# Kernel optimization log

Hardware: AMD Instinct MI355X
Metric: run time of the kernel (lower is better)

Reference implementation:

```python
import jax, jax.numpy as jnp
import numpy as np
from jax import lax

S = 48          # fixed crop size (original crops are ragged; fixed here for batching)
EPS = 0.1       # Sinkhorn entropic regularization
ITERS = 50      # Sinkhorn iterations
TINY = 1e-8


def setup_inputs() -> dict:
    key = jax.random.key(0)
    k1, k2, k3 = jax.random.split(key, 3)
    B, C, H, W = 16, 5, 160, 160
    hm_gt = jax.random.uniform(k1, (B, C, H, W), dtype=jnp.float32)
    hm_pred = jax.random.uniform(k2, (B, C, H, W), dtype=jnp.float32)
    tops = jax.random.randint(k3, (B, 8, 2), 0, 112, dtype=jnp.int32)  # (y, x) per rect
    return {"hm_gt": hm_gt, "hm_pred": hm_pred, "tops": tops}


def _geometry_distance(s):
    # pairwise Euclidean distance between pixel centers of an s x s crop -> [s*s, s*s]
    ys, xs = jnp.meshgrid(jnp.arange(s, dtype=jnp.float32),
                          jnp.arange(s, dtype=jnp.float32), indexing="ij")
    pts = jnp.stack([ys.ravel(), xs.ravel()], axis=-1)          # [s*s, 2]
    d2 = jnp.sum((pts[:, None, :] - pts[None, :, :]) ** 2, -1)  # [s*s, s*s]
    return jnp.sqrt(d2)


def _crop_all(hm, tops):
    # hm: [B, C, H, W], tops: [B, R, 2] -> crops [B, R, C, S, S]
    def crop_one(hm_b, top):  # hm_b [C,H,W], top [2]
        return lax.dynamic_slice(hm_b, (0, top[0], top[1]), (hm_b.shape[0], S, S))
    return jax.vmap(lambda hb, tb: jax.vmap(lambda t: crop_one(hb, t))(tb))(hm, tops)


def reference(hm_gt, hm_pred, tops):
    B, C, H, W = hm_gt.shape
    n = S * S
    dist = _geometry_distance(S)            # [n, n]
    K = jnp.exp(-dist / EPS)                # Gibbs kernel
    M = K * dist                            # for the transport cost readout

    a = _crop_all(hm_gt, tops).reshape(-1, n)    # [N, n]
    b = _crop_all(hm_pred, tops).reshape(-1, n)  # [N, n]
    a = a / (jnp.sum(a, -1, keepdims=True) + TINY)   # normalize to marginals
    b = b / (jnp.sum(b, -1, keepdims=True) + TINY)

    N = a.shape[0]
    u0 = jnp.full((N, n), 1.0 / n, dtype=a.dtype)
    v0 = jnp.full((N, n), 1.0 / n, dtype=a.dtype)

    def body(carry, _):
        u, v = carry
        v = b / (u @ K + TINY)      # [N,n] @ [n,n]
        u = a / (v @ K.T + TINY)
        return (u, v), None

    (u, v), _ = lax.scan(body, (u0, v0), None, length=ITERS)
    # loss per crop: sum_ij u_i K_ij dist_ij v_j
    loss = jnp.sum((u @ M) * v)
    return loss
```

## Files before the change

kernel.cpp:

```cpp
#include <hip/hip_runtime.h>

#define TINYF 1e-8f
#define NITER 50

__device__ __forceinline__ float bperm(int addr4, float v) {
    return __int_as_float(__builtin_amdgcn_ds_bpermute(addr4, __float_as_int(v)));
}
__device__ __forceinline__ float dpp_shr1(float v) {
    return __int_as_float(__builtin_amdgcn_update_dpp(0, __float_as_int(v), 0x111, 0xf, 0xf, true));
}
__device__ __forceinline__ float dpp_shl1(float v) {
    return __int_as_float(__builtin_amdgcn_update_dpp(0, __float_as_int(v), 0x101, 0xf, 0xf, true));
}

#define PREPF(C0_, C1_, C2_) \
    L2 = dpp_shr1(C1_); L1 = dpp_shr1(C2_); R1 = dpp_shl1(C0_); R2 = dpp_shl1(C1_); \
    s1a = L1 + C1_; s1b = C0_ + C2_; s1c = C1_ + R1; \
    s2a = L2 + C2_; s2b = L1 + R1; s2c = C0_ + R2;
#define PREPS(C0_, C1_, C2_) \
    L1 = dpp_shr1(C2_); R1 = dpp_shl1(C0_); \
    s1a = L1 + C1_; s1b = C0_ + C2_; s1c = C1_ + R1;
#define AT0(I, C0_, C1_, C2_, KA, KB, KC) \
    acc[I][0] += KA * C0_ + KB * s1a + KC * s2a; \
    acc[I][1] += KA * C1_ + KB * s1b + KC * s2b; \
    acc[I][2] += KA * C2_ + KB * s1c + KC * s2c;
#define AT0I(I, C0_, C1_, C2_, KA, KB, KC) \
    acc[I][0] = KA * C0_ + KB * s1a + KC * s2a; \
    acc[I][1] = KA * C1_ + KB * s1b + KC * s2b; \
    acc[I][2] = KA * C2_ + KB * s1c + KC * s2c;
#define AT1(I, C0_, C1_, C2_, KA, KB) \
    acc[I][0] += KA * C0_ + KB * s1a; \
    acc[I][1] += KA * C1_ + KB * s1b; \
    acc[I][2] += KA * C2_ + KB * s1c;
#define AT1I(I, C0_, C1_, C2_, KA, KB) \
    acc[I][0] = KA * C0_ + KB * s1a; \
    acc[I][1] = KA * C1_ + KB * s1b; \
    acc[I][2] = KA * C2_ + KB * s1c;
#define AT2(I, C0_, C1_, C2_, KA) \
    acc[I][0] += KA * C0_; \
    acc[I][1] += KA * C1_; \
    acc[I][2] += KA * C2_;
#define AT2I(I, C0_, C1_, C2_, KA) \
    acc[I][0] = KA * C0_; \
    acc[I][1] = KA * C1_; \
    acc[I][2] = KA * C2_;

__global__ void __launch_bounds__(128)
__attribute__((amdgpu_waves_per_eu(1, 2)))
sinkhorn_ft(const float* __restrict__ hm_gt,
            const float* __restrict__ hm_pred,
            const int* __restrict__ tops,
            float* __restrict__ out) {
    __shared__ __align__(16) float EX[2 * 512];
    __shared__ float sred[4];

    const int t = threadIdx.x;
    const int W = t >> 6;
    const int l = t & 63;
    const int b = l >> 4, c = l & 15;
    const bool btop = (b == 0), bbot = (b == 3);
    const bool xchg = (W == 0) ? bbot : btop;
    const int upA = ((l - 16) & 63) << 2;
    const int dnA = ((l + 16) & 63) << 2;

    const int blk = blockIdx.x;
    const int bi = blk / 40, rr = (blk / 5) % 8, cc = blk % 5;
    const int y0 = tops[(bi * 8 + rr) * 2 + 0];
    const int x0 = tops[(bi * 8 + rr) * 2 + 1];
    const float* srcA = hm_gt + (size_t)(bi * 5 + cc) * 25600;
    const float* srcB = hm_pred + (size_t)(bi * 5 + cc) * 25600;

    float* wp = EX + W * 256 + c * 4;
    const float* rp = EX + (1 - W) * 256 + c * 4;

    float va[6][3], vb[6][3];
    float sA = 0.f, sB = 0.f;
    const int rbase = y0 + 24 * W + 6 * b;
#pragma unroll
    for (int i = 0; i < 6; ++i) {
        const int g = (rbase + i) * 160 + x0 + 3 * c;
#pragma unroll
        for (int j = 0; j < 3; ++j) {
            const float A = srcA[g + j];
            const float B = srcB[g + j];
            va[i][j] = A; vb[i][j] = B;
            sA += A; sB += B;
        }
    }
#pragma unroll
    for (int o = 1; o < 64; o <<= 1) {
        sA += __shfl_xor(sA, o, 64);
        sB += __shfl_xor(sB, o, 64);
    }
    if (l == 0) { sred[W] = sA; sred[2 + W] = sB; }
    __syncthreads();
    sA = sred[0] + sred[1];
    sB = sred[2] + sred[3];
    const float nA = 1.0f / (sA + TINYF);
    const float nB = 1.0f / (sB + TINYF);
#pragma unroll
    for (int i = 0; i < 6; ++i)
#pragma unroll
        for (int j = 0; j < 3; ++j) { va[i][j] *= nA; vb[i][j] *= nB; }

    const float e10 = expf(-1.0f / 0.1f);
    const float e2  = expf(-sqrtf(2.0f) / 0.1f);
    const float e20 = expf(-2.0f / 0.1f);

    float xu[6][3], xv[6][3], acc[6][3];
    const float u0 = 1.0f / 2304.0f;
#pragma unroll
    for (int i = 0; i < 6; ++i)
#pragma unroll
        for (int j = 0; j < 3; ++j) xu[i][j] = u0;

    if (xchg) {
        *(float4*)(wp)      = make_float4(u0, u0, u0, 0.f);
        *(float4*)(wp + 64) = make_float4(u0, u0, u0, 0.f);
    }
    __syncthreads();

    auto conv = [&](const float (&x)[6][3], int poffR,
                    float K00, float K01, float K02,
                    float K10, float K11, float K20) {
        float4 q0 = make_float4(0.f, 0.f, 0.f, 0.f), q1 = q0;
        if (xchg) {
            q0 = *(const float4*)(rp + poffR);
            q1 = *(const float4*)(rp + poffR + 64);
        }
        float tA[3], tB[3], tC[3], tD[3];
#pragma unroll
        for (int j = 0; j < 3; ++j) {
            tA[j] = bperm(upA, x[4][j]);
            tB[j] = bperm(upA, x[5][j]);
            tC[j] = bperm(dnA, x[0][j]);
            tD[j] = bperm(dnA, x[1][j]);
        }

        float L1, L2, R1, R2, s1a, s1b, s1c, s2a, s2b, s2c;
        PREPF(x[0][0], x[0][1], x[0][2])
        AT0I(0, x[0][0], x[0][1], x[0][2], K00, K01, K02)
        AT1I(1, x[0][0], x[0][1], x[0][2], K10, K11)
        AT2I(2, x[0][0], x[0][1], x[0][2], K20)
        PREPF(x[1][0], x[1][1], x[1][2])
        AT1(0, x[1][0], x[1][1], x[1][2], K10, K11)
        AT0(1, x[1][0], x[1][1], x[1][2], K00, K01, K02)
        AT1(2, x[1][0], x[1][1], x[1][2], K10, K11)
        AT2I(3, x[1][0], x[1][1], x[1][2], K20)
        PREPF(x[2][0], x[2][1], x[2][2])
        AT2(0, x[2][0], x[2][1], x[2][2], K20)
        AT1(1, x[2][0], x[2][1], x[2][2], K10, K11)
        AT0(2, x[2][0], x[2][1], x[2][2], K00, K01, K02)
        AT1(3, x[2][0], x[2][1], x[2][2], K10, K11)
        AT2I(4, x[2][0], x[2][1], x[2][2], K20)
        PREPF(x[3][0], x[3][1], x[3][2])
        AT2(1, x[3][0], x[3][1], x[3][2], K20)
        AT1(2, x[3][0], x[3][1], x[3][2], K10, K11)
        AT0(3, x[3][0], x[3][1], x[3][2], K00, K01, K02)
        AT1(4, x[3][0], x[3][1], x[3][2], K10, K11)
        AT2I(5, x[3][0], x[3][1], x[3][2], K20)
        PREPF(x[4][0], x[4][1], x[4][2])
        AT2(2, x[4][0], x[4][1], x[4][2], K20)
        AT1(3, x[4][0], x[4][1], x[4][2], K10, K11)
        AT0(4, x[4][0], x[4][1], x[4][2], K00, K01, K02)
        AT1(5, x[4][0], x[4][1], x[4][2], K10, K11)
        PREPF(x[5][0], x[5][1], x[5][2])
        AT2(3, x[5][0], x[5][1], x[5][2], K20)
        AT1(4, x[5][0], x[5][1], x[5][2], K10, K11)
        AT0(5, x[5][0], x[5][1], x[5][2], K00, K01, K02)

        float hA[3], hB[3], hC[3], hD[3];
        const float qv0[3] = {q0.x, q0.y, q0.z};
        const float qv1[3] = {q1.x, q1.y, q1.z};
#pragma unroll
        for (int j = 0; j < 3; ++j) {
            if (W == 0) {
                hA[j] = btop ? 0.f : tA[j];
                hB[j] = btop ? 0.f : tB[j];
                hC[j] = bbot ? qv0[j] : tC[j];
                hD[j] = bbot ? qv1[j] : tD[j];
            } else {
                hA[j] = btop ? qv0[j] : tA[j];
                hB[j] = btop ? qv1[j] : tB[j];
                hC[j] = bbot ? 0.f : tC[j];
                hD[j] = bbot ? 0.f : tD[j];
            }
        }
        PREPS(hB[0], hB[1], hB[2])
        AT1(0, hB[0], hB[1], hB[2], K10, K11)
        AT2(1, hB[0], hB[1], hB[2], K20)
        AT2(0, hA[0], hA[1], hA[2], K20)
        PREPS(hC[0], hC[1], hC[2])
        AT2(4, hC[0], hC[1], hC[2], K20)
        AT1(5, hC[0], hC[1], hC[2], K10, K11)
        AT2(5, hD[0], hD[1], hD[2], K20)
    };

    auto publish = [&](const float (&y)[6][3], int poffW) {
        if (xchg) {
            const int r0 = (W == 0) ? 4 : 0;
            *(float4*)(wp + poffW)      = make_float4(y[r0][0], y[r0][1], y[r0][2], 0.f);
            *(float4*)(wp + poffW + 64) = make_float4(y[r0+1][0], y[r0+1][1], y[r0+1][2], 0.f);
        }
        __syncthreads();
    };

#pragma unroll 1
    for (int it = 0; it < NITER; ++it) {
        conv(xu, 0, 1.0f, e10, e20, e10, e2, e20);
#pragma unroll
        for (int i = 0; i < 6; ++i)
#pragma unroll
            for (int j = 0; j < 3; ++j)
                xv[i][j] = vb[i][j] * __builtin_amdgcn_rcpf(acc[i][j] + TINYF);
        publish(xv, 512);

        conv(xv, 512, 1.0f, e10, e20, e10, e2, e20);
#pragma unroll
        for (int i = 0; i < 6; ++i)
#pragma unroll
            for (int j = 0; j < 3; ++j)
                xu[i][j] = va[i][j] * __builtin_amdgcn_rcpf(acc[i][j] + TINYF);
        publish(xu, 0);
    }

    const float s2f = sqrtf(2.0f);
    const float m01 = e10, m02 = e20 * 2.0f, m11 = e2 * s2f;
    conv(xu, 0, 0.0f, m01, m02, m01, m11, m02);
    float lsum = 0.f;
#pragma unroll
    for (int i = 0; i < 6; ++i)
#pragma unroll
        for (int j = 0; j < 3; ++j)
            lsum += acc[i][j] * xv[i][j];

#pragma unroll
    for (int o = 1; o < 64; o <<= 1) lsum += __shfl_xor(lsum, o, 64);
    if (l == 0) sred[W] = lsum;
    __syncthreads();
    if (t == 0) atomicAdd(out, sred[0] + sred[1]);
}

extern "C" void kernel_launch(void* const* d_in, const int* in_sizes, int n_in,
                              void* d_out, int out_size, void* d_ws, size_t ws_size,
                              hipStream_t stream) {
    (void)in_sizes; (void)n_in; (void)out_size; (void)d_ws; (void)ws_size;
    const float* hm_gt = (const float*)d_in[0];
    const float* hm_pred = (const float*)d_in[1];
    const int* tops = (const int*)d_in[2];
    float* out = (float*)d_out;

    hipMemsetAsync(out, 0, sizeof(float), stream);
    sinkhorn_ft<<<dim3(640), dim3(128), 0, stream>>>(hm_gt, hm_pred, tops, out);
}
```

Baseline: 184.0 us.

## Split convolution into interior and halo parts to overlap barrier with compute

The per-half-iteration convolution is split into an interior part that only needs the thread's own values plus cross-lane permutes, and a halo part that reads the neighbouring wave's rows from LDS. Each new vector is published to LDS, then the interior convolution runs before the barrier, and the halo contribution is added after it. The aim is to hide barrier and LDS-exchange latency behind the interior arithmetic instead of stalling on the barrier first. The final readout keeps a leftover first interior/halo pass with mismatched weights whose result is overwritten, so it adds a little redundant work.

```diff
diff --git a/kernel.cpp b/kernel.cpp
--- a/kernel.cpp
+++ b/kernel.cpp
@@ -47,10 +47,10 @@
 
 __global__ void __launch_bounds__(128)
 __attribute__((amdgpu_waves_per_eu(1, 2)))
-sinkhorn_ft(const float* __restrict__ hm_gt,
-            const float* __restrict__ hm_pred,
-            const int* __restrict__ tops,
-            float* __restrict__ out) {
+sinkhorn_shadow(const float* __restrict__ hm_gt,
+                const float* __restrict__ hm_pred,
+                const int* __restrict__ tops,
+                float* __restrict__ out) {
     __shared__ __align__(16) float EX[2 * 512];
     __shared__ float sred[4];
 
@@ -108,35 +108,32 @@
     const float e20 = expf(-2.0f / 0.1f);
 
     float xu[6][3], xv[6][3], acc[6][3];
+    float tA[3], tB[3], tC[3], tD[3];
     const float u0 = 1.0f / 2304.0f;
 #pragma unroll
     for (int i = 0; i < 6; ++i)
 #pragma unroll
         for (int j = 0; j < 3; ++j) xu[i][j] = u0;
 
-    if (xchg) {
-        *(float4*)(wp)      = make_float4(u0, u0, u0, 0.f);
-        *(float4*)(wp + 64) = make_float4(u0, u0, u0, 0.f);
-    }
-    __syncthreads();
-
-    auto conv = [&](const float (&x)[6][3], int poffR,
-                    float K00, float K01, float K02,
-                    float K10, float K11, float K20) {
-        float4 q0 = make_float4(0.f, 0.f, 0.f, 0.f), q1 = q0;
+    auto publish = [&](const float (&y)[6][3], int poffW) {
         if (xchg) {
-            q0 = *(const float4*)(rp + poffR);
-            q1 = *(const float4*)(rp + poffR + 64);
-        }
-        float tA[3], tB[3], tC[3], tD[3];
+            const int r0 = (W == 0) ? 4 : 0;
+            *(float4*)(wp + poffW)      = make_float4(y[r0][0], y[r0][1], y[r0][2], 0.f);
+            *(float4*)(wp + poffW + 64) = make_float4(y[r0+1][0], y[r0+1][1], y[r0+1][2], 0.f);
+        }
+    };
+    auto bcand = [&](const float (&y)[6][3]) {
 #pragma unroll
         for (int j = 0; j < 3; ++j) {
-            tA[j] = bperm(upA, x[4][j]);
-            tB[j] = bperm(upA, x[5][j]);
-            tC[j] = bperm(dnA, x[0][j]);
-            tD[j] = bperm(dnA, x[1][j]);
-        }
-
+            tA[j] = bperm(upA, y[4][j]);
+            tB[j] = bperm(upA, y[5][j]);
+            tC[j] = bperm(dnA, y[0][j]);
+            tD[j] = bperm(dnA, y[1][j]);
+        }
+    };
+    auto conv_own = [&](const float (&x)[6][3],
+                        float K00, float K01, float K02,
+                        float K10, float K11, float K20) {
         float L1, L2, R1, R2, s1a, s1b, s1c, s2a, s2b, s2c;
         PREPF(x[0][0], x[0][1], x[0][2])
         AT0I(0, x[0][0], x[0][1], x[0][2], K00, K01, K02)
@@ -168,7 +165,11 @@
         AT2(3, x[5][0], x[5][1], x[5][2], K20)
         AT1(4, x[5][0], x[5][1], x[5][2], K10, K11)
         AT0(5, x[5][0], x[5][1], x[5][2], K00, K01, K02)
-
+    };
+    auto conv_halo = [&](int poffR,
+                         float K10, float K11, float K20) {
+        const float4 q0 = *(const float4*)(rp + poffR);
+        const float4 q1 = *(const float4*)(rp + poffR + 64);
         float hA[3], hB[3], hC[3], hD[3];
         const float qv0[3] = {q0.x, q0.y, q0.z};
         const float qv1[3] = {q1.x, q1.y, q1.z};
@@ -186,6 +187,7 @@
                 hD[j] = bbot ? 0.f : tD[j];
             }
         }
+        float L1, R1, s1a, s1b, s1c;
         PREPS(hB[0], hB[1], hB[2])
         AT1(0, hB[0], hB[1], hB[2], K10, K11)
         AT2(1, hB[0], hB[1], hB[2], K20)
@@ -196,37 +198,44 @@
         AT2(5, hD[0], hD[1], hD[2], K20)
     };
 
-    auto publish = [&](const float (&y)[6][3], int poffW) {
-        if (xchg) {
-            const int r0 = (W == 0) ? 4 : 0;
-            *(float4*)(wp + poffW)      = make_float4(y[r0][0], y[r0][1], y[r0][2], 0.f);
-            *(float4*)(wp + poffW + 64) = make_float4(y[r0+1][0], y[r0+1][1], y[r0+1][2], 0.f);
-        }
-        __syncthreads();
-    };
+    publish(xu, 0);
+    bcand(xu);
+    conv_own(xu, 1.0f, e10, e20, e10, e2, e20);
+    __syncthreads();
 
 #pragma unroll 1
     for (int it = 0; it < NITER; ++it) {
-        conv(xu, 0, 1.0f, e10, e20, e10, e2, e20);
+        conv_halo(0, e10, e2, e20);
 #pragma unroll
         for (int i = 0; i < 6; ++i)
 #pragma unroll
             for (int j = 0; j < 3; ++j)
                 xv[i][j] = vb[i][j] * __builtin_amdgcn_rcpf(acc[i][j] + TINYF);
         publish(xv, 512);
-
-        conv(xv, 512, 1.0f, e10, e20, e10, e2, e20);
+        bcand(xv);
+        conv_own(xv, 1.0f, e10, e20, e10, e2, e20);
+        __syncthreads();
+
+        conv_halo(512, e10, e2, e20);
 #pragma unroll
         for (int i = 0; i < 6; ++i)
 #pragma unroll
             for (int j = 0; j < 3; ++j)
                 xu[i][j] = va[i][j] * __builtin_amdgcn_rcpf(acc[i][j] + TINYF);
         publish(xu, 0);
+        bcand(xu);
+        conv_own(xu, 1.0f, e10, e20, e10, e2, e20);
+        __syncthreads();
     }
 
     const float s2f = sqrtf(2.0f);
     const float m01 = e10, m02 = e20 * 2.0f, m11 = e2 * s2f;
-    conv(xu, 0, 0.0f, m01, m02, m01, m11, m02);
+    bcand(xu);
+    conv_own(xu, 0.0f, m01, m02, m01, m11, m02);
+    conv_halo(0, m11, 0.0f, m02);
+    bcand(xu);
+    conv_own(xu, 0.0f, m01, m02, m01, m11, m02);
+    conv_halo(0, m01, m11, m02);
     float lsum = 0.f;
 #pragma unroll
     for (int i = 0; i < 6; ++i)
@@ -251,5 +260,5 @@
     float* out = (float*)d_out;
 
     hipMemsetAsync(out, 0, sizeof(float), stream);
-    sinkhorn_ft<<<dim3(640), dim3(128), 0, stream>>>(hm_gt, hm_pred, tops, out);
-}
+    sinkhorn_shadow<<<dim3(640), dim3(128), 0, stream>>>(hm_gt, hm_pred, tops, out);
+}
```

After: 200.8 us. 9.1% more time.
